# Performance work log

Measured on AMD Instinct MI355X. Metric: run time of the kernel, lower is better.

The kernel has to match this reference:

```python
import jax, jax.numpy as jnp
import numpy as np

T, D, I, E, G, LG, K = 2048, 1024, 512, 32, 8, 4, 6
SI = 2 * I  # shared expert inter dim = n_shared_experts * inter_dim
ROUTE_SCALE = 1.0


def setup_inputs() -> dict:
    key = jax.random.key(0)
    ks = jax.random.split(key, 16)
    s = 0.02
    f = jnp.float32
    return {
        "x": jax.random.normal(ks[0], (T, D), f),
        "router_w": jax.random.normal(ks[1], (E, D), f) * s,
        "router_b": jax.random.normal(ks[2], (E,), f) * s,
        "W1": jax.random.normal(ks[3], (E, D, I), f) * s,
        "b1": jax.random.normal(ks[4], (E, I), f) * s,
        "W2": jax.random.normal(ks[5], (E, D, I), f) * s,
        "b2": jax.random.normal(ks[6], (E, I), f) * s,
        "W3": jax.random.normal(ks[7], (E, I, D), f) * s,
        "b3": jax.random.normal(ks[8], (E, D), f) * s,
        "sw1": jax.random.normal(ks[9], (D, SI), f) * s,
        "sb1": jax.random.normal(ks[10], (SI,), f) * s,
        "sw2": jax.random.normal(ks[11], (D, SI), f) * s,
        "sb2": jax.random.normal(ks[12], (SI,), f) * s,
        "sw3": jax.random.normal(ks[13], (SI, D), f) * s,
        "sb3": jax.random.normal(ks[14], (D,), f) * s,
    }


def _route(x, router_w, router_b):
    # Router: softmax scores (fp32), group-limited top-k.
    logits = x @ router_w.T + router_b                      # [T, E]
    scores = jax.nn.softmax(logits.astype(jnp.float32), axis=-1)
    original = scores
    sg = scores.reshape(x.shape[0], G, E // G)              # [T, G, E/G]
    # no router bias -> group score = sum of top-2 expert scores per group
    group_scores = jnp.sum(jax.lax.top_k(sg, 2)[0], axis=-1)  # [T, G]
    _, gidx = jax.lax.top_k(group_scores, LG)               # [T, LG]
    keep = jnp.zeros((x.shape[0], G), bool).at[jnp.arange(x.shape[0])[:, None], gidx].set(True)
    masked = jnp.where(keep[:, :, None], sg, -jnp.inf).reshape(x.shape[0], E)
    _, idx = jax.lax.top_k(masked, K)                       # [T, K]
    vals = jnp.take_along_axis(original, idx, axis=1) * ROUTE_SCALE
    return vals.astype(x.dtype), idx


def reference(x, router_w, router_b, W1, b1, W2, b2, W3, b3, sw1, sb1, sw2, sb2, sw3, sb3):
    vals, idx = _route(x, router_w, router_b)
    # dense gate matrix [T, E]; top-k indices per row are distinct
    gates = jnp.zeros((x.shape[0], E), x.dtype).at[jnp.arange(x.shape[0])[:, None], idx].set(vals)
    # routed experts: Expert(x) = W3 @ silu(w1(x) * w2(x))
    h1 = jnp.einsum('td,edi->tei', x, W1) + b1              # [T, E, I]
    h2 = jnp.einsum('td,edi->tei', x, W2) + b2
    h = jax.nn.silu(h1 * h2)
    y = jnp.einsum('tei,eid->td', h * gates[:, :, None], W3) + gates @ b3
    # shared expert
    z = jax.nn.silu((x @ sw1 + sb1) * (x @ sw2 + sb2)) @ sw3 + sb3
    return y + z
```

## Files before the change

kernel.cpp:

```cpp
#include <hip/hip_runtime.h>
#include <hip/hip_bf16.h>
#include <math.h>

#define T_CONST 2048
#define D_CONST 1024
#define I_CONST 512
#define SI_CONST 1024
#define E_CONST 32
#define G_CONST 8
#define LG_CONST 4
#define KSEL 6

typedef __attribute__((ext_vector_type(8))) short short8;
typedef __attribute__((ext_vector_type(4))) float floatx4;

__device__ inline unsigned pack_bf16(float a, float b) {
  __hip_bfloat162 h = __float22bfloat162_rn(float2{a, b});
  return *reinterpret_cast<unsigned*>(&h);
}

__device__ inline void gload16(const void* g, void* l) {
  __builtin_amdgcn_global_load_lds(
      (const __attribute__((address_space(1))) unsigned int*)g,
      (__attribute__((address_space(3))) unsigned int*)l, 16, 0, 0);
}

__global__ __launch_bounds__(256) void cvt_x(const float* __restrict__ in,
                                             __hip_bfloat16* __restrict__ out) {
  size_t i = ((size_t)blockIdx.x * 256 + threadIdx.x) * 4;
  float4 v = *(const float4*)&in[i];
  uint2 u{pack_bf16(v.x, v.y), pack_bf16(v.z, v.w)};
  *(uint2*)&out[i] = u;
}

__global__ __launch_bounds__(256) void cvt_rwt(const float* __restrict__ rw,
                                               float* __restrict__ rwt) {
  int i = blockIdx.x * 256 + threadIdx.x;
  int d = i >> 5, e = i & 31;
  rwt[d * 32 + e] = rw[e * D_CONST + d];
}

__global__ __launch_bounds__(256) void transpose_all(
    const float* __restrict__ W1, const float* __restrict__ W2,
    const float* __restrict__ W3, const float* __restrict__ sw1,
    const float* __restrict__ sw2, const float* __restrict__ sw3,
    __hip_bfloat16* __restrict__ W1t, __hip_bfloat16* __restrict__ W2t,
    __hip_bfloat16* __restrict__ W3t, __hip_bfloat16* __restrict__ sw1t,
    __hip_bfloat16* __restrict__ sw2t, __hip_bfloat16* __restrict__ sw3t) {
  __shared__ float tile[64][65];
  int b = blockIdx.x;
  const float* in;
  __hip_bfloat16* out;
  int K, N, k0, n0;
  if (b < 8192) {
    int local = b & 4095;
    int mat = local >> 7, rem = local & 127;
    K = 1024; N = 512;
    in = ((b < 4096) ? W1 : W2) + (size_t)mat * (1024 * 512);
    out = ((b < 4096) ? W1t : W2t) + (size_t)mat * (1024 * 512);
    n0 = (rem & 7) * 64; k0 = (rem >> 3) * 64;
  } else if (b < 12288) {
    int local = b - 8192;
    int mat = local >> 7, rem = local & 127;
    K = 512; N = 1024;
    in = W3 + (size_t)mat * (512 * 1024);
    out = W3t + (size_t)mat * (512 * 1024);
    n0 = (rem & 15) * 64; k0 = (rem >> 4) * 64;
  } else {
    int local = b - 12288;
    int which = local >> 8, rem = local & 255;
    K = 1024; N = 1024;
    in = which == 0 ? sw1 : which == 1 ? sw2 : sw3;
    out = which == 0 ? sw1t : which == 1 ? sw2t : sw3t;
    n0 = (rem & 15) * 64; k0 = (rem >> 4) * 64;
  }
  int tid = threadIdx.x;
  int tr = tid >> 4, tc4 = (tid & 15) * 4;
#pragma unroll
  for (int i = 0; i < 4; ++i) {
    float4 v = *(const float4*)&in[(size_t)(k0 + tr + 16 * i) * N + n0 + tc4];
    tile[tr + 16 * i][tc4 + 0] = v.x;
    tile[tr + 16 * i][tc4 + 1] = v.y;
    tile[tr + 16 * i][tc4 + 2] = v.z;
    tile[tr + 16 * i][tc4 + 3] = v.w;
  }
  __syncthreads();
#pragma unroll
  for (int i = 0; i < 4; ++i) {
    int n = tr + 16 * i;
    unsigned lo = pack_bf16(tile[tc4 + 0][n], tile[tc4 + 1][n]);
    unsigned hi = pack_bf16(tile[tc4 + 2][n], tile[tc4 + 3][n]);
    uint2 u{lo, hi};
    *(uint2*)&out[(size_t)(n0 + n) * K + k0 + tc4] = u;
  }
}

__global__ __launch_bounds__(256) void router2(
    const float* __restrict__ x, const float* __restrict__ rwt,
    const float* __restrict__ rb, int* __restrict__ counts,
    int* __restrict__ stok, float* __restrict__ gatel) {
  const int lane = threadIdx.x & 63;
  const int wv = threadIdx.x >> 6;
  const int t = blockIdx.x * 4 + wv;
  const int e = lane & 31, h = lane >> 5;
  const float* xp = x + (size_t)t * D_CONST;
  float s = 0.f;
#pragma unroll 8
  for (int d = h; d < D_CONST; d += 2) s = fmaf(xp[d], rwt[d * 32 + e], s);
  s += __shfl_xor(s, 32);
  s += rb[e];
  float mx = s;
#pragma unroll
  for (int m = 16; m >= 1; m >>= 1) mx = fmaxf(mx, __shfl_xor(mx, m));
  float p = expf(s - mx);
  float sum = p;
#pragma unroll
  for (int m = 16; m >= 1; m >>= 1) sum += __shfl_xor(sum, m);
  float sc = p / sum;
  float a = sc, bb = __shfl_xor(a, 1);
  float hi = fmaxf(a, bb), lo = fminf(a, bb);
  float oh = __shfl_xor(hi, 2), ol = __shfl_xor(lo, 2);
  float gs = fmaxf(fmaxf(hi + oh, hi + lo), oh + ol);
  const int g = e >> 2;
  unsigned keep = 0;
  float gv = gs;
#pragma unroll
  for (int r = 0; r < LG_CONST; ++r) {
    float v = gv;
    int gi = g;
#pragma unroll
    for (int m = 16; m >= 1; m >>= 1) {
      float ov = __shfl_xor(v, m);
      int og = __shfl_xor(gi, m);
      if (ov > v || (ov == v && og < gi)) { v = ov; gi = og; }
    }
    keep |= 1u << gi;
    if (g == gi) gv = -1e30f;
  }
  float cand = ((keep >> g) & 1u) ? sc : -1e30f;
  int sel_e = -1;
  float sel_v = 0.f;
#pragma unroll
  for (int r = 0; r < KSEL; ++r) {
    float v = cand;
    int ei = e;
#pragma unroll
    for (int m = 16; m >= 1; m >>= 1) {
      float ov = __shfl_xor(v, m);
      int oe = __shfl_xor(ei, m);
      if (ov > v || (ov == v && oe < ei)) { v = ov; ei = oe; }
    }
    if (lane == r) { sel_e = ei; sel_v = v; }
    if (e == ei) cand = -1e30f;
  }
  if (lane < KSEL) {
    int pos = atomicAdd(&counts[sel_e], 1);
    stok[sel_e * T_CONST + pos] = t;
    gatel[sel_e * T_CONST + pos] = sel_v;
  }
}

__global__ void scan_k(const int* __restrict__ counts, int* __restrict__ offsets) {
  if (threadIdx.x == 0) {
    int s = 0;
    for (int e = 0; e < E_CONST; ++e) { offsets[e] = s; s += counts[e]; }
    offsets[E_CONST] = s;
  }
}

__global__ __launch_bounds__(256) void gather_x(
    const __hip_bfloat16* __restrict__ xbf, const int* __restrict__ counts,
    const int* __restrict__ offsets, const int* __restrict__ stok,
    const float* __restrict__ gatel, __hip_bfloat16* __restrict__ Xg,
    int* __restrict__ ctok, float* __restrict__ cgate) {
  int e = blockIdx.x;
  int cnt = counts[e];
  int row = blockIdx.y * 16 + (threadIdx.x >> 4);
  if (row >= cnt) return;
  int seg = threadIdx.x & 15;
  int tok = stok[e * T_CONST + row];
  int dst = offsets[e] + row;
  const uint4* src = (const uint4*)(xbf + (size_t)tok * D_CONST);
  uint4* d = (uint4*)(Xg + (size_t)dst * D_CONST);
#pragma unroll
  for (int i = 0; i < 8; ++i) d[i * 16 + seg] = src[i * 16 + seg];
  if (seg == 0) { ctok[dst] = tok; cgate[dst] = gatel[e * T_CONST + row]; }
}

__global__ __launch_bounds__(256, 2) void up_fused(
    const __hip_bfloat16* __restrict__ Xg, const __hip_bfloat16* __restrict__ xbf,
    const __hip_bfloat16* __restrict__ W1t, const __hip_bfloat16* __restrict__ W2t,
    const __hip_bfloat16* __restrict__ sw1t, const __hip_bfloat16* __restrict__ sw2t,
    const float* __restrict__ b1, const float* __restrict__ b2,
    const float* __restrict__ sb1, const float* __restrict__ sb2,
    const int* __restrict__ counts, const int* __restrict__ offsets,
    __hip_bfloat16* __restrict__ He, __hip_bfloat16* __restrict__ Hs) {
  const int z = blockIdx.z;
  const bool SH = (z == E_CONST);
  const int N = SH ? SI_CONST : I_CONST;
  const int n0 = blockIdx.x * 128;
  if (n0 >= N) return;
  const int cnt = SH ? T_CONST : counts[z];
  const int m0 = blockIdx.y * 128;
  if (m0 >= cnt) return;
  const int base = SH ? 0 : offsets[z];

  const __hip_bfloat16* Ab = SH ? (xbf + (size_t)m0 * D_CONST)
                                : (Xg + (size_t)(base + m0) * D_CONST);
  const __hip_bfloat16* B1 = SH ? (sw1t + (size_t)n0 * D_CONST)
                                : (W1t + ((size_t)z * I_CONST + n0) * D_CONST);
  const __hip_bfloat16* B2 = SH ? (sw2t + (size_t)n0 * D_CONST)
                                : (W2t + ((size_t)z * I_CONST + n0) * D_CONST);

  __shared__ short As[8192], Bs1[8192], Bs2[8192];

  const int tid = threadIdx.x, lane = tid & 63, wv = tid >> 6;
  const int l15 = lane & 15, quad = lane >> 4;
  const int wm = wv & 1, wn = wv >> 1;
  const int lr = lane >> 3, lc = lane & 7, kap = lc ^ lr;

  const __hip_bfloat16 *aG[4], *b1G[4], *b2G[4];
#pragma unroll
  for (int i = 0; i < 4; ++i) {
    int r = (wv * 4 + i) * 8 + lr;
    aG[i] = Ab + (size_t)r * D_CONST + kap * 8;
    b1G[i] = B1 + (size_t)r * D_CONST + kap * 8;
    b2G[i] = B2 + (size_t)r * D_CONST + kap * 8;
  }
  const int ldsu = (wv * 4 * 64 + lane) * 8;

  floatx4 acc1[4][4] = {};
  floatx4 acc2[4][4] = {};

  for (int it = 0; it < D_CONST / 64; ++it) {
#pragma unroll
    for (int i = 0; i < 4; ++i) {
      gload16(aG[i], &As[ldsu + i * 512]);
      gload16(b1G[i], &Bs1[ldsu + i * 512]);
      gload16(b2G[i], &Bs2[ldsu + i * 512]);
      aG[i] += 64; b1G[i] += 64; b2G[i] += 64;
    }
    __syncthreads();
#pragma unroll
    for (int c = 0; c < 2; ++c) {
      const int kc = c * 4 + quad;
      short8 a[4], x1[4], x2[4];
#pragma unroll
      for (int mi = 0; mi < 4; ++mi) {
        int m = wm * 64 + mi * 16 + l15;
        a[mi] = *(const short8*)&As[(m * 8 + (kc ^ (m & 7))) * 8];
      }
#pragma unroll
      for (int ni = 0; ni < 4; ++ni) {
        int n = wn * 64 + ni * 16 + l15;
        int u = (n * 8 + (kc ^ (n & 7))) * 8;
        x1[ni] = *(const short8*)&Bs1[u];
        x2[ni] = *(const short8*)&Bs2[u];
      }
#pragma unroll
      for (int mi = 0; mi < 4; ++mi)
#pragma unroll
        for (int ni = 0; ni < 4; ++ni) {
          acc1[mi][ni] = __builtin_amdgcn_mfma_f32_16x16x32_bf16(a[mi], x1[ni], acc1[mi][ni], 0, 0, 0);
          acc2[mi][ni] = __builtin_amdgcn_mfma_f32_16x16x32_bf16(a[mi], x2[ni], acc2[mi][ni], 0, 0, 0);
        }
    }
    __syncthreads();
  }

  const float* pb1 = SH ? sb1 : (b1 + (size_t)z * I_CONST);
  const float* pb2 = SH ? sb2 : (b2 + (size_t)z * I_CONST);
  __hip_bfloat16* outp = SH ? (Hs + (size_t)m0 * SI_CONST + n0)
                            : (He + (size_t)(base + m0) * I_CONST + n0);
  const int ldo = SH ? SI_CONST : I_CONST;
  float c1[4], c2[4];
#pragma unroll
  for (int ni = 0; ni < 4; ++ni) {
    int n = wn * 64 + ni * 16 + l15;
    c1[ni] = pb1[n0 + n];
    c2[ni] = pb2[n0 + n];
  }
#pragma unroll
  for (int mi = 0; mi < 4; ++mi) {
#pragma unroll
    for (int reg = 0; reg < 4; ++reg) {
      int m = wm * 64 + mi * 16 + quad * 4 + reg;
      if (m0 + m >= cnt) continue;
#pragma unroll
      for (int ni = 0; ni < 4; ++ni) {
        int n = wn * 64 + ni * 16 + l15;
        float h1 = acc1[mi][ni][reg] + c1[ni];
        float h2 = acc2[mi][ni][reg] + c2[ni];
        float p = h1 * h2;
        float s = p / (1.f + expf(-p));
        outp[(size_t)m * ldo + n] = __float2bfloat16(s);
      }
    }
  }
}

__global__ __launch_bounds__(256, 3) void down_fused(
    const __hip_bfloat16* __restrict__ He, const __hip_bfloat16* __restrict__ Hs,
    const __hip_bfloat16* __restrict__ W3t, const __hip_bfloat16* __restrict__ sw3t,
    const float* __restrict__ b3, const float* __restrict__ sb3,
    const int* __restrict__ counts, const int* __restrict__ offsets,
    const int* __restrict__ ctok, const float* __restrict__ cgate,
    float* __restrict__ out) {
  const int z = blockIdx.z;
  const bool SH = (z == E_CONST);
  const int n0 = blockIdx.x * 128;
  const int cnt = SH ? T_CONST : counts[z];
  const int m0 = blockIdx.y * 128;
  if (m0 >= cnt) return;
  const int base = SH ? 0 : offsets[z];
  const int Kd = SH ? SI_CONST : I_CONST;

  const __hip_bfloat16* Ab = SH ? (Hs + (size_t)m0 * SI_CONST)
                                : (He + (size_t)(base + m0) * I_CONST);
  const __hip_bfloat16* Bb = SH ? (sw3t + (size_t)n0 * SI_CONST)
                                : (W3t + ((size_t)z * D_CONST + n0) * I_CONST);

  __shared__ short As[8192], Bs[8192];

  const int tid = threadIdx.x, lane = tid & 63, wv = tid >> 6;
  const int l15 = lane & 15, quad = lane >> 4;
  const int wm = wv & 1, wn = wv >> 1;
  const int lr = lane >> 3, lc = lane & 7, kap = lc ^ lr;

  const __hip_bfloat16 *aG[4], *bG[4];
#pragma unroll
  for (int i = 0; i < 4; ++i) {
    int r = (wv * 4 + i) * 8 + lr;
    aG[i] = Ab + (size_t)r * Kd + kap * 8;
    bG[i] = Bb + (size_t)r * Kd + kap * 8;
  }
  const int ldsu = (wv * 4 * 64 + lane) * 8;

  floatx4 acc[4][4] = {};
  const int kiter = Kd / 64;

  for (int it = 0; it < kiter; ++it) {
#pragma unroll
    for (int i = 0; i < 4; ++i) {
      gload16(aG[i], &As[ldsu + i * 512]);
      gload16(bG[i], &Bs[ldsu + i * 512]);
      aG[i] += 64; bG[i] += 64;
    }
    __syncthreads();
#pragma unroll
    for (int c = 0; c < 2; ++c) {
      const int kc = c * 4 + quad;
      short8 a[4], bbf[4];
#pragma unroll
      for (int mi = 0; mi < 4; ++mi) {
        int m = wm * 64 + mi * 16 + l15;
        a[mi] = *(const short8*)&As[(m * 8 + (kc ^ (m & 7))) * 8];
      }
#pragma unroll
      for (int ni = 0; ni < 4; ++ni) {
        int n = wn * 64 + ni * 16 + l15;
        bbf[ni] = *(const short8*)&Bs[(n * 8 + (kc ^ (n & 7))) * 8];
      }
#pragma unroll
      for (int mi = 0; mi < 4; ++mi)
#pragma unroll
        for (int ni = 0; ni < 4; ++ni)
          acc[mi][ni] = __builtin_amdgcn_mfma_f32_16x16x32_bf16(a[mi], bbf[ni], acc[mi][ni], 0, 0, 0);
    }
    __syncthreads();
  }

  float bias[4];
#pragma unroll
  for (int ni = 0; ni < 4; ++ni) {
    int n = n0 + wn * 64 + ni * 16 + l15;
    bias[ni] = SH ? sb3[n] : b3[(size_t)z * D_CONST + n];
  }
#pragma unroll
  for (int mi = 0; mi < 4; ++mi) {
#pragma unroll
    for (int reg = 0; reg < 4; ++reg) {
      int m = wm * 64 + mi * 16 + quad * 4 + reg;
      if (m0 + m >= cnt) continue;
      int tok;
      float gate;
      if (SH) { tok = m0 + m; gate = 1.f; }
      else { int grow = base + m0 + m; tok = ctok[grow]; gate = cgate[grow]; }
#pragma unroll
      for (int ni = 0; ni < 4; ++ni) {
        int n = n0 + wn * 64 + ni * 16 + l15;
        float v = gate * (acc[mi][ni][reg] + bias[ni]);
        atomicAdd(&out[(size_t)tok * D_CONST + n], v);
      }
    }
  }
}

extern "C" void kernel_launch(void* const* d_in, const int* in_sizes, int n_in,
                              void* d_out, int out_size, void* d_ws, size_t ws_size,
                              hipStream_t stream) {
  const float* x   = (const float*)d_in[0];
  const float* rw  = (const float*)d_in[1];
  const float* rb  = (const float*)d_in[2];
  const float* W1  = (const float*)d_in[3];
  const float* b1  = (const float*)d_in[4];
  const float* W2  = (const float*)d_in[5];
  const float* b2  = (const float*)d_in[6];
  const float* W3  = (const float*)d_in[7];
  const float* b3  = (const float*)d_in[8];
  const float* sw1 = (const float*)d_in[9];
  const float* sb1 = (const float*)d_in[10];
  const float* sw2 = (const float*)d_in[11];
  const float* sb2 = (const float*)d_in[12];
  const float* sw3 = (const float*)d_in[13];
  const float* sb3 = (const float*)d_in[14];
  float* out = (float*)d_out;

  char* w = (char*)d_ws;
  size_t off = 0;
  auto alloc = [&](size_t bytes) {
    char* p = w + off;
    off += (bytes + 255) & ~(size_t)255;
    return p;
  };
  int* counts = (int*)alloc(E_CONST * 4);
  int* offsets = (int*)alloc((E_CONST + 1) * 4);
  int* stok = (int*)alloc((size_t)E_CONST * T_CONST * 4);
  float* gatel = (float*)alloc((size_t)E_CONST * T_CONST * 4);
  float* rwt = (float*)alloc((size_t)D_CONST * E_CONST * 4);
  int* ctok = (int*)alloc((size_t)T_CONST * KSEL * 4);
  float* cgate = (float*)alloc((size_t)T_CONST * KSEL * 4);
  __hip_bfloat16* x_bf = (__hip_bfloat16*)alloc((size_t)T_CONST * D_CONST * 2);
  __hip_bfloat16* Xg = (__hip_bfloat16*)alloc((size_t)(T_CONST * KSEL + 128) * D_CONST * 2);
  __hip_bfloat16* W1t = (__hip_bfloat16*)alloc((size_t)E_CONST * D_CONST * I_CONST * 2);
  __hip_bfloat16* W2t = (__hip_bfloat16*)alloc((size_t)E_CONST * D_CONST * I_CONST * 2);
  __hip_bfloat16* W3t = (__hip_bfloat16*)alloc((size_t)E_CONST * I_CONST * D_CONST * 2);
  __hip_bfloat16* sw1t = (__hip_bfloat16*)alloc((size_t)D_CONST * SI_CONST * 2);
  __hip_bfloat16* sw2t = (__hip_bfloat16*)alloc((size_t)D_CONST * SI_CONST * 2);
  __hip_bfloat16* sw3t = (__hip_bfloat16*)alloc((size_t)SI_CONST * D_CONST * 2);
  __hip_bfloat16* He = (__hip_bfloat16*)alloc((size_t)(T_CONST * KSEL + 128) * I_CONST * 2);
  __hip_bfloat16* Hs = (__hip_bfloat16*)alloc((size_t)T_CONST * SI_CONST * 2);

  hipMemsetAsync(counts, 0, E_CONST * sizeof(int), stream);
  hipMemsetAsync(out, 0, (size_t)out_size * sizeof(float), stream);
  cvt_rwt<<<(D_CONST * E_CONST) / 256, 256, 0, stream>>>(rw, rwt);
  cvt_x<<<(T_CONST * D_CONST) / 1024, 256, 0, stream>>>(x, x_bf);
  transpose_all<<<13056, 256, 0, stream>>>(W1, W2, W3, sw1, sw2, sw3,
                                           W1t, W2t, W3t, sw1t, sw2t, sw3t);
  router2<<<T_CONST / 4, 256, 0, stream>>>(x, rwt, rb, counts, stok, gatel);
  scan_k<<<1, 64, 0, stream>>>(counts, offsets);
  gather_x<<<dim3(E_CONST, T_CONST / 16), 256, 0, stream>>>(
      x_bf, counts, offsets, stok, gatel, Xg, ctok, cgate);
  up_fused<<<dim3(8, 16, E_CONST + 1), 256, 0, stream>>>(
      Xg, x_bf, W1t, W2t, sw1t, sw2t, b1, b2, sb1, sb2, counts, offsets, He, Hs);
  down_fused<<<dim3(8, 16, E_CONST + 1), 256, 0, stream>>>(
      He, Hs, W3t, sw3t, b3, sb3, counts, offsets, ctok, cgate, out);
}
```

Baseline: 502.6 us.

## Triple-buffer LDS with async global loads in both expert GEMM kernels

Both grouped GEMM kernels move from a single-buffered BK=64 loop with two syncthreads per step to a 3-slot ring of BK=32 LDS tiles. Tiles are prefetched two steps ahead with global_load_lds, and explicit vmcnt waits plus raw barriers let the next loads overlap the MFMA work. The LDS swizzle is changed to match the 32-wide rows, and s_setprio is raised around the MFMA block. The gain depends on the hand-counted vmcnt values being correct. The smaller K step also means more barriers per tile.

```diff
diff --git a/kernel.cpp b/kernel.cpp
--- a/kernel.cpp
+++ b/kernel.cpp
@@ -10,6 +10,7 @@
 #define G_CONST 8
 #define LG_CONST 4
 #define KSEL 6
+#define BK 32
 
 typedef __attribute__((ext_vector_type(8))) short short8;
 typedef __attribute__((ext_vector_type(4))) float floatx4;
@@ -212,61 +213,76 @@
   const __hip_bfloat16* B2 = SH ? (sw2t + (size_t)n0 * D_CONST)
                                 : (W2t + ((size_t)z * I_CONST + n0) * D_CONST);
 
-  __shared__ short As[8192], Bs1[8192], Bs2[8192];
+  __shared__ short As[3 * 4096], Bs1[3 * 4096], Bs2[3 * 4096];
 
   const int tid = threadIdx.x, lane = tid & 63, wv = tid >> 6;
   const int l15 = lane & 15, quad = lane >> 4;
   const int wm = wv & 1, wn = wv >> 1;
-  const int lr = lane >> 3, lc = lane & 7, kap = lc ^ lr;
-
-  const __hip_bfloat16 *aG[4], *b1G[4], *b2G[4];
-#pragma unroll
-  for (int i = 0; i < 4; ++i) {
-    int r = (wv * 4 + i) * 8 + lr;
-    aG[i] = Ab + (size_t)r * D_CONST + kap * 8;
+  const int lr = lane >> 2;
+  const int lc = lane & 3;
+
+  const __hip_bfloat16 *aG[2], *b1G[2], *b2G[2];
+#pragma unroll
+  for (int i = 0; i < 2; ++i) {
+    int r = wv * 32 + i * 16 + lr;
+    int kap = lc ^ ((r >> 1) & 3);
+    aG[i]  = Ab + (size_t)r * D_CONST + kap * 8;
     b1G[i] = B1 + (size_t)r * D_CONST + kap * 8;
     b2G[i] = B2 + (size_t)r * D_CONST + kap * 8;
   }
-  const int ldsu = (wv * 4 * 64 + lane) * 8;
+  const int ldsu = wv * 1024 + lane * 8;
 
   floatx4 acc1[4][4] = {};
   floatx4 acc2[4][4] = {};
 
-  for (int it = 0; it < D_CONST / 64; ++it) {
-#pragma unroll
-    for (int i = 0; i < 4; ++i) {
-      gload16(aG[i], &As[ldsu + i * 512]);
-      gload16(b1G[i], &Bs1[ldsu + i * 512]);
-      gload16(b2G[i], &Bs2[ldsu + i * 512]);
-      aG[i] += 64; b1G[i] += 64; b2G[i] += 64;
-    }
-    __syncthreads();
-#pragma unroll
-    for (int c = 0; c < 2; ++c) {
-      const int kc = c * 4 + quad;
-      short8 a[4], x1[4], x2[4];
-#pragma unroll
-      for (int mi = 0; mi < 4; ++mi) {
-        int m = wm * 64 + mi * 16 + l15;
-        a[mi] = *(const short8*)&As[(m * 8 + (kc ^ (m & 7))) * 8];
+  const int nIter = D_CONST / BK;
+
+  auto stage = [&](int slot, int kk) {
+    const int sb = slot * 4096;
+#pragma unroll
+    for (int i = 0; i < 2; ++i) {
+      gload16(aG[i] + kk,  &As [sb + ldsu + i * 512]);
+      gload16(b1G[i] + kk, &Bs1[sb + ldsu + i * 512]);
+      gload16(b2G[i] + kk, &Bs2[sb + ldsu + i * 512]);
+    }
+  };
+
+  stage(0, 0);
+  stage(1, BK);
+  int sl0 = 0, sl1 = 1, sl2 = 2;
+
+  for (int s = 0; s < nIter; ++s) {
+    int kn = (s + 2 < nIter) ? (s + 2) * BK : (nIter - 1) * BK;
+    stage(sl2, kn);
+    asm volatile("s_waitcnt vmcnt(12)" ::: "memory");
+    __builtin_amdgcn_s_barrier();
+    const int sb = sl0 * 4096;
+    short8 a[4], x1[4], x2[4];
+#pragma unroll
+    for (int mi = 0; mi < 4; ++mi) {
+      int m = wm * 64 + mi * 16 + l15;
+      a[mi] = *(const short8*)&As[sb + m * 32 + (quad ^ ((m >> 1) & 3)) * 8];
+    }
+#pragma unroll
+    for (int ni = 0; ni < 4; ++ni) {
+      int n = wn * 64 + ni * 16 + l15;
+      int u = sb + n * 32 + (quad ^ ((n >> 1) & 3)) * 8;
+      x1[ni] = *(const short8*)&Bs1[u];
+      x2[ni] = *(const short8*)&Bs2[u];
+    }
+    __builtin_amdgcn_s_setprio(1);
+#pragma unroll
+    for (int mi = 0; mi < 4; ++mi)
+#pragma unroll
+      for (int ni = 0; ni < 4; ++ni) {
+        acc1[mi][ni] = __builtin_amdgcn_mfma_f32_16x16x32_bf16(a[mi], x1[ni], acc1[mi][ni], 0, 0, 0);
+        acc2[mi][ni] = __builtin_amdgcn_mfma_f32_16x16x32_bf16(a[mi], x2[ni], acc2[mi][ni], 0, 0, 0);
       }
-#pragma unroll
-      for (int ni = 0; ni < 4; ++ni) {
-        int n = wn * 64 + ni * 16 + l15;
-        int u = (n * 8 + (kc ^ (n & 7))) * 8;
-        x1[ni] = *(const short8*)&Bs1[u];
-        x2[ni] = *(const short8*)&Bs2[u];
-      }
-#pragma unroll
-      for (int mi = 0; mi < 4; ++mi)
-#pragma unroll
-        for (int ni = 0; ni < 4; ++ni) {
-          acc1[mi][ni] = __builtin_amdgcn_mfma_f32_16x16x32_bf16(a[mi], x1[ni], acc1[mi][ni], 0, 0, 0);
-          acc2[mi][ni] = __builtin_amdgcn_mfma_f32_16x16x32_bf16(a[mi], x2[ni], acc2[mi][ni], 0, 0, 0);
-        }
-    }
-    __syncthreads();
-  }
+    __builtin_amdgcn_s_setprio(0);
+    __builtin_amdgcn_s_barrier();
+    int t = sl0; sl0 = sl1; sl1 = sl2; sl2 = t;
+  }
+  asm volatile("s_waitcnt vmcnt(0)" ::: "memory");
 
   const float* pb1 = SH ? sb1 : (b1 + (size_t)z * I_CONST);
   const float* pb2 = SH ? sb2 : (b2 + (size_t)z * I_CONST);
@@ -320,55 +336,67 @@
   const __hip_bfloat16* Bb = SH ? (sw3t + (size_t)n0 * SI_CONST)
                                 : (W3t + ((size_t)z * D_CONST + n0) * I_CONST);
 
-  __shared__ short As[8192], Bs[8192];
+  __shared__ short As[3 * 4096], Bs[3 * 4096];
 
   const int tid = threadIdx.x, lane = tid & 63, wv = tid >> 6;
   const int l15 = lane & 15, quad = lane >> 4;
   const int wm = wv & 1, wn = wv >> 1;
-  const int lr = lane >> 3, lc = lane & 7, kap = lc ^ lr;
-
-  const __hip_bfloat16 *aG[4], *bG[4];
-#pragma unroll
-  for (int i = 0; i < 4; ++i) {
-    int r = (wv * 4 + i) * 8 + lr;
+  const int lr = lane >> 2, lc = lane & 3;
+
+  const __hip_bfloat16 *aG[2], *bG[2];
+#pragma unroll
+  for (int i = 0; i < 2; ++i) {
+    int r = wv * 32 + i * 16 + lr;
+    int kap = lc ^ ((r >> 1) & 3);
     aG[i] = Ab + (size_t)r * Kd + kap * 8;
     bG[i] = Bb + (size_t)r * Kd + kap * 8;
   }
-  const int ldsu = (wv * 4 * 64 + lane) * 8;
+  const int ldsu = wv * 1024 + lane * 8;
 
   floatx4 acc[4][4] = {};
-  const int kiter = Kd / 64;
-
-  for (int it = 0; it < kiter; ++it) {
-#pragma unroll
-    for (int i = 0; i < 4; ++i) {
-      gload16(aG[i], &As[ldsu + i * 512]);
-      gload16(bG[i], &Bs[ldsu + i * 512]);
-      aG[i] += 64; bG[i] += 64;
-    }
-    __syncthreads();
-#pragma unroll
-    for (int c = 0; c < 2; ++c) {
-      const int kc = c * 4 + quad;
-      short8 a[4], bbf[4];
-#pragma unroll
-      for (int mi = 0; mi < 4; ++mi) {
-        int m = wm * 64 + mi * 16 + l15;
-        a[mi] = *(const short8*)&As[(m * 8 + (kc ^ (m & 7))) * 8];
-      }
-#pragma unroll
-      for (int ni = 0; ni < 4; ++ni) {
-        int n = wn * 64 + ni * 16 + l15;
-        bbf[ni] = *(const short8*)&Bs[(n * 8 + (kc ^ (n & 7))) * 8];
-      }
-#pragma unroll
-      for (int mi = 0; mi < 4; ++mi)
-#pragma unroll
-        for (int ni = 0; ni < 4; ++ni)
-          acc[mi][ni] = __builtin_amdgcn_mfma_f32_16x16x32_bf16(a[mi], bbf[ni], acc[mi][ni], 0, 0, 0);
-    }
-    __syncthreads();
-  }
+  const int nIter = Kd / BK;
+
+  auto stage = [&](int slot, int kk) {
+    const int sb = slot * 4096;
+#pragma unroll
+    for (int i = 0; i < 2; ++i) {
+      gload16(aG[i] + kk, &As[sb + ldsu + i * 512]);
+      gload16(bG[i] + kk, &Bs[sb + ldsu + i * 512]);
+    }
+  };
+
+  stage(0, 0);
+  stage(1, BK);
+  int sl0 = 0, sl1 = 1, sl2 = 2;
+
+  for (int s = 0; s < nIter; ++s) {
+    int kn = (s + 2 < nIter) ? (s + 2) * BK : (nIter - 1) * BK;
+    stage(sl2, kn);
+    asm volatile("s_waitcnt vmcnt(8)" ::: "memory");
+    __builtin_amdgcn_s_barrier();
+    const int sb = sl0 * 4096;
+    short8 a[4], bbf[4];
+#pragma unroll
+    for (int mi = 0; mi < 4; ++mi) {
+      int m = wm * 64 + mi * 16 + l15;
+      a[mi] = *(const short8*)&As[sb + m * 32 + (quad ^ ((m >> 1) & 3)) * 8];
+    }
+#pragma unroll
+    for (int ni = 0; ni < 4; ++ni) {
+      int n = wn * 64 + ni * 16 + l15;
+      bbf[ni] = *(const short8*)&Bs[sb + n * 32 + (quad ^ ((n >> 1) & 3)) * 8];
+    }
+    __builtin_amdgcn_s_setprio(1);
+#pragma unroll
+    for (int mi = 0; mi < 4; ++mi)
+#pragma unroll
+      for (int ni = 0; ni < 4; ++ni)
+        acc[mi][ni] = __builtin_amdgcn_mfma_f32_16x16x32_bf16(a[mi], bbf[ni], acc[mi][ni], 0, 0, 0);
+    __builtin_amdgcn_s_setprio(0);
+    __builtin_amdgcn_s_barrier();
+    int t = sl0; sl0 = sl1; sl1 = sl2; sl2 = t;
+  }
+  asm volatile("s_waitcnt vmcnt(0)" ::: "memory");
 
   float bias[4];
 #pragma unroll
```

New measurement: 526.3 us. +4.7%, slower.
